# Kernel tuning notes

Measured on AMD Instinct MI355X. Metric: run time of the kernel, lower is better.

The kernel has to match this reference:

```python
import jax, jax.numpy as jnp
import numpy as np

B, H, S, D = 4, 16, 2048, 128

def setup_inputs() -> dict:
    key = jax.random.key(0)
    kq, kk, kv = jax.random.split(key, 3)
    q = jax.random.normal(kq, (B, H, S, D), dtype=jnp.float32)
    k = jax.random.normal(kk, (B, H, S, D), dtype=jnp.float32)
    v = jax.random.normal(kv, (B, H, S, D), dtype=jnp.float32)
    return {"q": q, "k": k, "v": v}

def reference(q, k, v):
    # scores: [B, H, S, S] -- NOTE: original module applies no 1/sqrt(D) scale
    scores = jnp.einsum("bhqd,bhkd->bhqk", q, k)
    a = jax.nn.softmax(scores, axis=-1)  # numerically stable softmax
    return jnp.einsum("bhqk,bhkd->bhqd", a, v)
```

## Files before the change

kernel.cpp:

```cpp
#include <hip/hip_runtime.h>
#include <hip/hip_bf16.h>


#define QBLK   64
#define KVBLK  64
#define DHEAD  128
#define SEQ    2048
#define KPAD   136
#define PPAD   72

typedef _Float16 f16x8 __attribute__((ext_vector_type(8)));
typedef _Float16 f16x4 __attribute__((ext_vector_type(4)));
typedef float    f32x4 __attribute__((ext_vector_type(4)));

#define AS1P(x) ((const __attribute__((address_space(1))) void*)(size_t)(x))
#define AS3P(x) ((__attribute__((address_space(3))) void*)(unsigned long long)(unsigned)(size_t)(x))

__global__ __launch_bounds__(256)
void preconv_kernel(const float* __restrict__ K, const float* __restrict__ V,
                    _Float16* __restrict__ Kp, _Float16* __restrict__ Vp) {
    const int bt = blockIdx.x;
    const size_t src = (size_t)bt * (KVBLK * DHEAD);
    const float* Kt = K + src;
    const float* Vt = V + src;
    _Float16* Ko = Kp + src;
    _Float16* Vo = Vp + src;
    #pragma unroll
    for (int j = 0; j < 4; ++j) {
        const int c = threadIdx.x + 256 * j;
        {
            const int row = c >> 4;
            const int d0  = (c & 15) * 8;
            float4 f0 = *(const float4*)(Kt + row * DHEAD + d0);
            float4 f1 = *(const float4*)(Kt + row * DHEAD + d0 + 4);
            f16x8 h;
            h[0]=(_Float16)f0.x; h[1]=(_Float16)f0.y; h[2]=(_Float16)f0.z; h[3]=(_Float16)f0.w;
            h[4]=(_Float16)f1.x; h[5]=(_Float16)f1.y; h[6]=(_Float16)f1.z; h[7]=(_Float16)f1.w;
            *(f16x8*)&Ko[row * 128 + (d0 ^ ((row & 7) << 3))] = h;
        }
        {
            const int d   = c & 127;
            const int kvg = c >> 7;
            f16x8 h;
            #pragma unroll
            for (int i = 0; i < 8; ++i)
                h[i] = (_Float16)Vt[(kvg * 8 + i) * DHEAD + d];
            *(f16x8*)&Vo[d * 64 + ((kvg * 8) ^ ((d & 7) << 3))] = h;
        }
    }
}

__global__ __launch_bounds__(256, 3)
void attn_fwd_kernel(const float* __restrict__ Q, const _Float16* __restrict__ Kp,
                     const _Float16* __restrict__ Vp, float* __restrict__ O) {
    __shared__ __align__(16) _Float16 K_lds[KVBLK * DHEAD];
    __shared__ __align__(16) _Float16 V_lds[DHEAD * KVBLK];
    __shared__ __align__(16) _Float16 P_lds[4 * 16 * 64];

    const int tid  = threadIdx.x;
    const int lane = tid & 63;
    const int wave = tid >> 6;
    const int g    = lane >> 4;
    const int lg   = lane & 15;

    const int flat    = blockIdx.x + gridDim.x * blockIdx.y;
    const int newflat = (flat & 7) * 256 + (flat >> 3);
    const int qtile   = newflat & 31;
    const int bh      = newflat >> 5;

    const float* Qg = Q + (size_t)bh * SEQ * DHEAD + (size_t)(qtile * QBLK) * DHEAD;
    float*       Og = O + (size_t)bh * SEQ * DHEAD + (size_t)(qtile * QBLK) * DHEAD;

    f16x8 qf[4];
    {
        const float* qrow = Qg + (size_t)(wave * 16 + lg) * DHEAD;
        #pragma unroll
        for (int dc = 0; dc < 4; ++dc) {
            const int d0 = dc * 32 + g * 8;
            float4 f0 = *(const float4*)(qrow + d0);
            float4 f1 = *(const float4*)(qrow + d0 + 4);
            qf[dc][0] = (_Float16)f0.x; qf[dc][1] = (_Float16)f0.y;
            qf[dc][2] = (_Float16)f0.z; qf[dc][3] = (_Float16)f0.w;
            qf[dc][4] = (_Float16)f1.x; qf[dc][5] = (_Float16)f1.y;
            qf[dc][6] = (_Float16)f1.z; qf[dc][7] = (_Float16)f1.w;
        }
    }

    f32x4 acc[8];
    #pragma unroll
    for (int dt = 0; dt < 8; ++dt) { acc[dt][0]=0.f; acc[dt][1]=0.f; acc[dt][2]=0.f; acc[dt][3]=0.f; }
    float m = -1e30f, l = 0.f;

    for (int t = 0; t < SEQ / KVBLK; ++t) {
        {
            const _Float16* Ktile = Kp + (size_t)(bh * 32 + t) * (KVBLK * DHEAD);
            const _Float16* Vtile = Vp + (size_t)(bh * 32 + t) * (KVBLK * DHEAD);
            #pragma unroll
            for (int i = 0; i < 4; ++i) {
                const int eoff = wave * 2048 + i * 512;
                __builtin_amdgcn_global_load_lds(AS1P(Ktile + eoff + lane * 8),
                                                 AS3P(&K_lds[eoff]), 16, 0, 0);
                __builtin_amdgcn_global_load_lds(AS1P(Vtile + eoff + lane * 8),
                                                 AS3P(&V_lds[eoff]), 16, 0, 0);
            }
        }
        __syncthreads();

        f32x4 s[4];
        __builtin_amdgcn_s_setprio(1);
        #pragma unroll
        for (int ct = 0; ct < 4; ++ct) {
            f32x4 a; a[0]=0.f; a[1]=0.f; a[2]=0.f; a[3]=0.f;
            #pragma unroll
            for (int dc = 0; dc < 4; ++dc) {
                const int krow = ct * 16 + lg;
                const int off  = krow * 128 + ((dc * 32 + g * 8) ^ ((krow & 7) << 3));
                f16x8 kh = *(const f16x8*)&K_lds[off];
                a = __builtin_amdgcn_mfma_f32_16x16x32_f16(kh, qf[dc], a, 0, 0, 0);
            }
            s[ct] = a;
        }
        __builtin_amdgcn_s_setprio(0);

        float pmax = s[0][0];
        #pragma unroll
        for (int ct = 0; ct < 4; ++ct)
            #pragma unroll
            for (int r = 0; r < 4; ++r)
                pmax = fmaxf(pmax, s[ct][r]);
        pmax = fmaxf(pmax, __shfl_xor(pmax, 16));
        pmax = fmaxf(pmax, __shfl_xor(pmax, 32));
        const float mnew = fmaxf(m, pmax);
        const float sc   = __expf(m - mnew);
        m = mnew;
        float rs = 0.f;
        #pragma unroll
        for (int ct = 0; ct < 4; ++ct)
            #pragma unroll
            for (int r = 0; r < 4; ++r) {
                float p = __expf(s[ct][r] - mnew);
                s[ct][r] = p;
                rs += p;
            }
        rs += __shfl_xor(rs, 16);
        rs += __shfl_xor(rs, 32);
        l = l * sc + rs;

        #pragma unroll
        for (int r = 0; r < 4; ++r) {
            const float scr = __shfl(sc, g * 20 + r);
            #pragma unroll
            for (int dt = 0; dt < 8; ++dt) acc[dt][r] *= scr;
        }

        _Float16* pbase = &P_lds[wave * 16 * 64];
        #pragma unroll
        for (int ct = 0; ct < 4; ++ct) {
            f16x4 pk;
            pk[0] = (_Float16)s[ct][0]; pk[1] = (_Float16)s[ct][1];
            pk[2] = (_Float16)s[ct][2]; pk[3] = (_Float16)s[ct][3];
            *(f16x4*)&pbase[lg * 64 + ((ct * 16 + g * 4) ^ ((lg & 7) << 3))] = pk;
        }

        __builtin_amdgcn_s_setprio(1);
        #pragma unroll
        for (int kt = 0; kt < 2; ++kt) {
            const int koff = (kt * 32 + g * 8) ^ ((lg & 7) << 3);
            f16x8 pf = *(const f16x8*)&pbase[lg * 64 + koff];
            #pragma unroll
            for (int dt = 0; dt < 8; ++dt) {
                f16x8 vf = *(const f16x8*)&V_lds[(dt * 16 + lg) * 64 + koff];
                acc[dt] = __builtin_amdgcn_mfma_f32_16x16x32_f16(pf, vf, acc[dt], 0, 0, 0);
            }
        }
        __builtin_amdgcn_s_setprio(0);
        __syncthreads();
    }

    const float linv = 1.f / l;
    float inv[4];
    #pragma unroll
    for (int r = 0; r < 4; ++r) inv[r] = __shfl(linv, g * 20 + r);
    float* ob = Og + (size_t)(wave * 16) * DHEAD;
    #pragma unroll
    for (int dt = 0; dt < 8; ++dt)
        #pragma unroll
        for (int r = 0; r < 4; ++r)
            ob[(size_t)(g * 4 + r) * DHEAD + dt * 16 + lg] = acc[dt][r] * inv[r];
}

__global__ __launch_bounds__(256, 3)
void attn_fwd_legacy(const float* __restrict__ Q, const float* __restrict__ K,
                     const float* __restrict__ V, float* __restrict__ O) {
    __shared__ __align__(16) _Float16 K_lds[KVBLK * KPAD];
    __shared__ __align__(16) _Float16 V_lds[KVBLK * DHEAD];
    __shared__ __align__(16) _Float16 P_lds[4 * 16 * PPAD];

    const int tid  = threadIdx.x;
    const int lane = tid & 63;
    const int wave = tid >> 6;
    const int g    = lane >> 4;
    const int lg   = lane & 15;

    const int flat    = blockIdx.x + gridDim.x * blockIdx.y;
    const int newflat = (flat & 7) * 256 + (flat >> 3);
    const int qtile   = newflat & 31;
    const int bh      = newflat >> 5;

    const size_t base = (size_t)bh * SEQ * DHEAD;
    const float* Qg = Q + base + (size_t)(qtile * QBLK) * DHEAD;
    const float* Kg = K + base;
    const float* Vg = V + base;
    float*       Og = O + base + (size_t)(qtile * QBLK) * DHEAD;

    const unsigned trbase = (unsigned)(size_t)&V_lds[0] + (unsigned)(g * 2048 + lg * 8);

    f16x8 qf[4];
    {
        const float* qrow = Qg + (size_t)(wave * 16 + lg) * DHEAD;
        #pragma unroll
        for (int dc = 0; dc < 4; ++dc) {
            const int d0 = dc * 32 + g * 8;
            float4 f0 = *(const float4*)(qrow + d0);
            float4 f1 = *(const float4*)(qrow + d0 + 4);
            qf[dc][0] = (_Float16)f0.x; qf[dc][1] = (_Float16)f0.y;
            qf[dc][2] = (_Float16)f0.z; qf[dc][3] = (_Float16)f0.w;
            qf[dc][4] = (_Float16)f1.x; qf[dc][5] = (_Float16)f1.y;
            qf[dc][6] = (_Float16)f1.z; qf[dc][7] = (_Float16)f1.w;
        }
    }

    f32x4 acc[8];
    #pragma unroll
    for (int dt = 0; dt < 8; ++dt) { acc[dt][0]=0.f; acc[dt][1]=0.f; acc[dt][2]=0.f; acc[dt][3]=0.f; }
    float m = -1e30f, l = 0.f;

    for (int t = 0; t < SEQ / KVBLK; ++t) {
        {
            const float* Kt = Kg + (size_t)t * KVBLK * DHEAD;
            #pragma unroll
            for (int j = 0; j < 4; ++j) {
                const int c   = tid + 256 * j;
                const int row = c >> 4;
                const int dc  = (c & 15) * 8;
                float4 f0 = *(const float4*)(Kt + row * DHEAD + dc);
                float4 f1 = *(const float4*)(Kt + row * DHEAD + dc + 4);
                f16x8 vh;
                vh[0]=(_Float16)f0.x; vh[1]=(_Float16)f0.y; vh[2]=(_Float16)f0.z; vh[3]=(_Float16)f0.w;
                vh[4]=(_Float16)f1.x; vh[5]=(_Float16)f1.y; vh[6]=(_Float16)f1.z; vh[7]=(_Float16)f1.w;
                *(f16x8*)&K_lds[row * KPAD + dc] = vh;
            }
            const float* Vt = Vg + (size_t)t * KVBLK * DHEAD;
            #pragma unroll
            for (int j = 0; j < 4; ++j) {
                const int c   = tid + 256 * j;
                const int d8  = (c & 1) | (((c >> 3) & 7) << 1);
                const int row = ((c >> 1) & 3) | ((c >> 6) << 2);
                const int d0  = d8 * 8;
                float4 f0 = *(const float4*)(Vt + row * DHEAD + d0);
                float4 f1 = *(const float4*)(Vt + row * DHEAD + d0 + 4);
                f16x8 vv;
                vv[0]=(_Float16)f0.x; vv[1]=(_Float16)f0.y; vv[2]=(_Float16)f0.z; vv[3]=(_Float16)f0.w;
                vv[4]=(_Float16)f1.x; vv[5]=(_Float16)f1.y; vv[6]=(_Float16)f1.z; vv[7]=(_Float16)f1.w;
                const int st = (row >> 2) * 8 + (d0 >> 4);
                *(f16x8*)&V_lds[st * 64 + (row & 3) * 16 + (d0 & 15)] = vv;
            }
        }
        __syncthreads();

        f32x4 s[4];
        __builtin_amdgcn_s_setprio(1);
        #pragma unroll
        for (int ct = 0; ct < 4; ++ct) {
            f32x4 a; a[0]=0.f; a[1]=0.f; a[2]=0.f; a[3]=0.f;
            #pragma unroll
            for (int dc = 0; dc < 4; ++dc) {
                const int off = (ct * 16 + lg) * KPAD + dc * 32 + g * 8;
                f16x8 kh = *(const f16x8*)&K_lds[off];
                a = __builtin_amdgcn_mfma_f32_16x16x32_f16(kh, qf[dc], a, 0, 0, 0);
            }
            s[ct] = a;
        }
        __builtin_amdgcn_s_setprio(0);

        float pmax = s[0][0];
        #pragma unroll
        for (int ct = 0; ct < 4; ++ct)
            #pragma unroll
            for (int r = 0; r < 4; ++r)
                pmax = fmaxf(pmax, s[ct][r]);
        pmax = fmaxf(pmax, __shfl_xor(pmax, 16));
        pmax = fmaxf(pmax, __shfl_xor(pmax, 32));
        const float mnew = fmaxf(m, pmax);
        const float sc   = __expf(m - mnew);
        m = mnew;
        float rs = 0.f;
        #pragma unroll
        for (int ct = 0; ct < 4; ++ct)
            #pragma unroll
            for (int r = 0; r < 4; ++r) {
                float p = __expf(s[ct][r] - mnew);
                s[ct][r] = p;
                rs += p;
            }
        rs += __shfl_xor(rs, 16);
        rs += __shfl_xor(rs, 32);
        l = l * sc + rs;

        #pragma unroll
        for (int r = 0; r < 4; ++r) {
            const float scr = __shfl(sc, g * 20 + r);
            #pragma unroll
            for (int dt = 0; dt < 8; ++dt) acc[dt][r] *= scr;
        }

        _Float16* pbase = &P_lds[wave * 16 * PPAD];
        #pragma unroll
        for (int ct = 0; ct < 4; ++ct) {
            f16x4 pk;
            pk[0] = (_Float16)s[ct][0]; pk[1] = (_Float16)s[ct][1];
            pk[2] = (_Float16)s[ct][2]; pk[3] = (_Float16)s[ct][3];
            *(f16x4*)&pbase[lg * PPAD + ct * 16 + g * 4] = pk;
        }

        #pragma unroll
        for (int kt = 0; kt < 2; ++kt) {
            f16x8 pf = *(const f16x8*)&pbase[lg * PPAD + kt * 32 + g * 8];
            #pragma unroll
            for (int dp = 0; dp < 4; ++dp) {
                f16x4 a0, a1, b0, b1;
                asm volatile(
                    "ds_read_b64_tr_b16 %0, %4 offset:%5\n\t"
                    "ds_read_b64_tr_b16 %1, %4 offset:%6\n\t"
                    "ds_read_b64_tr_b16 %2, %4 offset:%7\n\t"
                    "ds_read_b64_tr_b16 %3, %4 offset:%8\n\t"
                    "s_waitcnt lgkmcnt(0)"
                    : "=&v"(a0), "=&v"(a1), "=&v"(b0), "=&v"(b1)
                    : "v"(trbase),
                      "i"(kt * 8192 + (dp * 2 + 0) * 128),
                      "i"(kt * 8192 + 1024 + (dp * 2 + 0) * 128),
                      "i"(kt * 8192 + (dp * 2 + 1) * 128),
                      "i"(kt * 8192 + 1024 + (dp * 2 + 1) * 128)
                    : "memory");
                __builtin_amdgcn_sched_barrier(0);
                f16x8 vf0 = __builtin_shufflevector(a0, a1, 0, 1, 2, 3, 4, 5, 6, 7);
                f16x8 vf1 = __builtin_shufflevector(b0, b1, 0, 1, 2, 3, 4, 5, 6, 7);
                __builtin_amdgcn_s_setprio(1);
                acc[dp * 2 + 0] = __builtin_amdgcn_mfma_f32_16x16x32_f16(pf, vf0, acc[dp * 2 + 0], 0, 0, 0);
                acc[dp * 2 + 1] = __builtin_amdgcn_mfma_f32_16x16x32_f16(pf, vf1, acc[dp * 2 + 1], 0, 0, 0);
                __builtin_amdgcn_s_setprio(0);
            }
        }
        __syncthreads();
    }

    const float linv = 1.f / l;
    float inv[4];
    #pragma unroll
    for (int r = 0; r < 4; ++r) inv[r] = __shfl(linv, g * 20 + r);
    float* ob = Og + (size_t)(wave * 16) * DHEAD;
    #pragma unroll
    for (int dt = 0; dt < 8; ++dt)
        #pragma unroll
        for (int r = 0; r < 4; ++r)
            ob[(size_t)(g * 4 + r) * DHEAD + dt * 16 + lg] = acc[dt][r] * inv[r];
}

extern "C" void kernel_launch(void* const* d_in, const int* in_sizes, int n_in,
                              void* d_out, int out_size, void* d_ws, size_t ws_size,
                              hipStream_t stream) {
    const float* q = (const float*)d_in[0];
    const float* k = (const float*)d_in[1];
    const float* v = (const float*)d_in[2];
    float* out = (float*)d_out;
    const int BH = in_sizes[0] / (SEQ * DHEAD);
    dim3 grid(SEQ / QBLK, BH);

    const size_t elems = (size_t)BH * SEQ * DHEAD;
    const size_t need  = elems * 2 * sizeof(_Float16);
    if (ws_size >= need) {
        _Float16* Kp = (_Float16*)d_ws;
        _Float16* Vp = Kp + elems;
        preconv_kernel<<<dim3(BH * (SEQ / KVBLK)), dim3(256), 0, stream>>>(k, v, Kp, Vp);
        attn_fwd_kernel<<<grid, dim3(256), 0, stream>>>(q, Kp, Vp, out);
    } else {
        attn_fwd_legacy<<<grid, dim3(256), 0, stream>>>(q, k, v, out);
    }
}
```

Before: 250.8 us.

## Double-buffer K/V LDS tiles and skip online-softmax rescale below threshold

Splits K and V into two LDS buffers so the next tile's global-to-LDS load is issued before computing the current tile, overlapping memory traffic with MFMA work. The main loop is manually unrolled by two over the buffers. It also adds a lazy rescale: the running max and accumulator rescale are only updated when a new row max exceeds the old one by more than a threshold, saving exps and multiplies. LDS use doubles, so occupancy drops from 3 to 2 blocks per CU, and skipping rescales allows exponent values up to e^8 in fp16 P, which is a mild numerical risk.

```diff
diff --git a/kernel.cpp b/kernel.cpp
--- a/kernel.cpp
+++ b/kernel.cpp
@@ -6,8 +6,10 @@
 #define KVBLK  64
 #define DHEAD  128
 #define SEQ    2048
+#define NT     (SEQ / KVBLK)
 #define KPAD   136
 #define PPAD   72
+#define RESCALE_THR 8.0f
 
 typedef _Float16 f16x8 __attribute__((ext_vector_type(8)));
 typedef _Float16 f16x4 __attribute__((ext_vector_type(4)));
@@ -50,11 +52,11 @@
     }
 }
 
-__global__ __launch_bounds__(256, 3)
+__global__ __launch_bounds__(256, 2)
 void attn_fwd_kernel(const float* __restrict__ Q, const _Float16* __restrict__ Kp,
                      const _Float16* __restrict__ Vp, float* __restrict__ O) {
-    __shared__ __align__(16) _Float16 K_lds[KVBLK * DHEAD];
-    __shared__ __align__(16) _Float16 V_lds[DHEAD * KVBLK];
+    __shared__ __align__(16) _Float16 K_lds[2][KVBLK * DHEAD];
+    __shared__ __align__(16) _Float16 V_lds[2][KVBLK * DHEAD];
     __shared__ __align__(16) _Float16 P_lds[4 * 16 * 64];
 
     const int tid  = threadIdx.x;
@@ -91,91 +93,105 @@
     for (int dt = 0; dt < 8; ++dt) { acc[dt][0]=0.f; acc[dt][1]=0.f; acc[dt][2]=0.f; acc[dt][3]=0.f; }
     float m = -1e30f, l = 0.f;
 
-    for (int t = 0; t < SEQ / KVBLK; ++t) {
-        {
-            const _Float16* Ktile = Kp + (size_t)(bh * 32 + t) * (KVBLK * DHEAD);
-            const _Float16* Vtile = Vp + (size_t)(bh * 32 + t) * (KVBLK * DHEAD);
-            #pragma unroll
-            for (int i = 0; i < 4; ++i) {
-                const int eoff = wave * 2048 + i * 512;
-                __builtin_amdgcn_global_load_lds(AS1P(Ktile + eoff + lane * 8),
-                                                 AS3P(&K_lds[eoff]), 16, 0, 0);
-                __builtin_amdgcn_global_load_lds(AS1P(Vtile + eoff + lane * 8),
-                                                 AS3P(&V_lds[eoff]), 16, 0, 0);
-            }
-        }
+    #define STAGE(B, T) {                                                          \
+        const _Float16* Ktile = Kp + (size_t)(bh * 32 + (T)) * (KVBLK * DHEAD);    \
+        const _Float16* Vtile = Vp + (size_t)(bh * 32 + (T)) * (KVBLK * DHEAD);    \
+        _Pragma("unroll")                                                          \
+        for (int i = 0; i < 4; ++i) {                                              \
+            const int eoff = wave * 2048 + i * 512;                                \
+            __builtin_amdgcn_global_load_lds(AS1P(Ktile + eoff + lane * 8),        \
+                                             AS3P(&K_lds[B][eoff]), 16, 0, 0);     \
+            __builtin_amdgcn_global_load_lds(AS1P(Vtile + eoff + lane * 8),        \
+                                             AS3P(&V_lds[B][eoff]), 16, 0, 0);     \
+        }                                                                          \
+    }
+
+    #define COMPUTE(B) {                                                           \
+        f32x4 s[4];                                                                \
+        __builtin_amdgcn_s_setprio(1);                                             \
+        _Pragma("unroll")                                                          \
+        for (int ct = 0; ct < 4; ++ct) {                                           \
+            f32x4 a; a[0]=0.f; a[1]=0.f; a[2]=0.f; a[3]=0.f;                       \
+            _Pragma("unroll")                                                      \
+            for (int dc = 0; dc < 4; ++dc) {                                       \
+                const int krow = ct * 16 + lg;                                     \
+                const int koff2 = krow * 128 + ((dc * 32 + g * 8) ^ ((krow & 7) << 3)); \
+                f16x8 kh = *(const f16x8*)&K_lds[B][koff2];                        \
+                a = __builtin_amdgcn_mfma_f32_16x16x32_f16(kh, qf[dc], a, 0, 0, 0);\
+            }                                                                      \
+            s[ct] = a;                                                             \
+        }                                                                          \
+        __builtin_amdgcn_s_setprio(0);                                             \
+        float pmax = s[0][0];                                                      \
+        _Pragma("unroll")                                                          \
+        for (int ct = 0; ct < 4; ++ct)                                             \
+            _Pragma("unroll")                                                      \
+            for (int r = 0; r < 4; ++r)                                            \
+                pmax = fmaxf(pmax, s[ct][r]);                                      \
+        pmax = fmaxf(pmax, __shfl_xor(pmax, 16));                                  \
+        pmax = fmaxf(pmax, __shfl_xor(pmax, 32));                                  \
+        if (!__all(pmax - m <= RESCALE_THR)) {                                     \
+            const float mnew = fmaxf(m, pmax);                                     \
+            const float sc   = __expf(m - mnew);                                   \
+            m = mnew;                                                              \
+            l *= sc;                                                               \
+            _Pragma("unroll")                                                      \
+            for (int r = 0; r < 4; ++r) {                                          \
+                const float scr = __shfl(sc, g * 20 + r);                          \
+                _Pragma("unroll")                                                  \
+                for (int dt = 0; dt < 8; ++dt) acc[dt][r] *= scr;                  \
+            }                                                                      \
+        }                                                                          \
+        float rs = 0.f;                                                            \
+        _Pragma("unroll")                                                          \
+        for (int ct = 0; ct < 4; ++ct)                                             \
+            _Pragma("unroll")                                                      \
+            for (int r = 0; r < 4; ++r) {                                          \
+                float p = __expf(s[ct][r] - m);                                    \
+                s[ct][r] = p;                                                      \
+                rs += p;                                                           \
+            }                                                                      \
+        rs += __shfl_xor(rs, 16);                                                  \
+        rs += __shfl_xor(rs, 32);                                                  \
+        l += rs;                                                                   \
+        _Float16* pbase = &P_lds[wave * 16 * 64];                                  \
+        _Pragma("unroll")                                                          \
+        for (int ct = 0; ct < 4; ++ct) {                                           \
+            f16x4 pk;                                                              \
+            pk[0] = (_Float16)s[ct][0]; pk[1] = (_Float16)s[ct][1];                \
+            pk[2] = (_Float16)s[ct][2]; pk[3] = (_Float16)s[ct][3];                \
+            *(f16x4*)&pbase[lg * 64 + ((ct * 16 + g * 4) ^ ((lg & 7) << 3))] = pk; \
+        }                                                                          \
+        __builtin_amdgcn_s_setprio(1);                                             \
+        _Pragma("unroll")                                                          \
+        for (int kt = 0; kt < 2; ++kt) {                                           \
+            const int koff = (kt * 32 + g * 8) ^ ((lg & 7) << 3);                  \
+            f16x8 pf = *(const f16x8*)&pbase[lg * 64 + koff];                      \
+            _Pragma("unroll")                                                      \
+            for (int dt = 0; dt < 8; ++dt) {                                       \
+                f16x8 vf = *(const f16x8*)&V_lds[B][(dt * 16 + lg) * 64 + koff];   \
+                acc[dt] = __builtin_amdgcn_mfma_f32_16x16x32_f16(pf, vf, acc[dt], 0, 0, 0); \
+            }                                                                      \
+        }                                                                          \
+        __builtin_amdgcn_s_setprio(0);                                             \
+    }
+
+    STAGE(0, 0);
+    __syncthreads();
+
+    #pragma unroll 1
+    for (int tt = 0; tt < NT / 2; ++tt) {
+        const int t0 = tt * 2;
+        STAGE(1, t0 + 1);
+        COMPUTE(0);
         __syncthreads();
-
-        f32x4 s[4];
-        __builtin_amdgcn_s_setprio(1);
-        #pragma unroll
-        for (int ct = 0; ct < 4; ++ct) {
-            f32x4 a; a[0]=0.f; a[1]=0.f; a[2]=0.f; a[3]=0.f;
-            #pragma unroll
-            for (int dc = 0; dc < 4; ++dc) {
-                const int krow = ct * 16 + lg;
-                const int off  = krow * 128 + ((dc * 32 + g * 8) ^ ((krow & 7) << 3));
-                f16x8 kh = *(const f16x8*)&K_lds[off];
-                a = __builtin_amdgcn_mfma_f32_16x16x32_f16(kh, qf[dc], a, 0, 0, 0);
-            }
-            s[ct] = a;
-        }
-        __builtin_amdgcn_s_setprio(0);
-
-        float pmax = s[0][0];
-        #pragma unroll
-        for (int ct = 0; ct < 4; ++ct)
-            #pragma unroll
-            for (int r = 0; r < 4; ++r)
-                pmax = fmaxf(pmax, s[ct][r]);
-        pmax = fmaxf(pmax, __shfl_xor(pmax, 16));
-        pmax = fmaxf(pmax, __shfl_xor(pmax, 32));
-        const float mnew = fmaxf(m, pmax);
-        const float sc   = __expf(m - mnew);
-        m = mnew;
-        float rs = 0.f;
-        #pragma unroll
-        for (int ct = 0; ct < 4; ++ct)
-            #pragma unroll
-            for (int r = 0; r < 4; ++r) {
-                float p = __expf(s[ct][r] - mnew);
-                s[ct][r] = p;
-                rs += p;
-            }
-        rs += __shfl_xor(rs, 16);
-        rs += __shfl_xor(rs, 32);
-        l = l * sc + rs;
-
-        #pragma unroll
-        for (int r = 0; r < 4; ++r) {
-            const float scr = __shfl(sc, g * 20 + r);
-            #pragma unroll
-            for (int dt = 0; dt < 8; ++dt) acc[dt][r] *= scr;
-        }
-
-        _Float16* pbase = &P_lds[wave * 16 * 64];
-        #pragma unroll
-        for (int ct = 0; ct < 4; ++ct) {
-            f16x4 pk;
-            pk[0] = (_Float16)s[ct][0]; pk[1] = (_Float16)s[ct][1];
-            pk[2] = (_Float16)s[ct][2]; pk[3] = (_Float16)s[ct][3];
-            *(f16x4*)&pbase[lg * 64 + ((ct * 16 + g * 4) ^ ((lg & 7) << 3))] = pk;
-        }
-
-        __builtin_amdgcn_s_setprio(1);
-        #pragma unroll
-        for (int kt = 0; kt < 2; ++kt) {
-            const int koff = (kt * 32 + g * 8) ^ ((lg & 7) << 3);
-            f16x8 pf = *(const f16x8*)&pbase[lg * 64 + koff];
-            #pragma unroll
-            for (int dt = 0; dt < 8; ++dt) {
-                f16x8 vf = *(const f16x8*)&V_lds[(dt * 16 + lg) * 64 + koff];
-                acc[dt] = __builtin_amdgcn_mfma_f32_16x16x32_f16(pf, vf, acc[dt], 0, 0, 0);
-            }
-        }
-        __builtin_amdgcn_s_setprio(0);
+        if (t0 + 2 < NT) STAGE(0, t0 + 2);
+        COMPUTE(1);
         __syncthreads();
     }
+
+    #undef STAGE
+    #undef COMPUTE
 
     const float linv = 1.f / l;
     float inv[4];
@@ -235,7 +251,7 @@
     for (int dt = 0; dt < 8; ++dt) { acc[dt][0]=0.f; acc[dt][1]=0.f; acc[dt][2]=0.f; acc[dt][3]=0.f; }
     float m = -1e30f, l = 0.f;
 
-    for (int t = 0; t < SEQ / KVBLK; ++t) {
+    for (int t = 0; t < NT; ++t) {
         {
             const float* Kt = Kg + (size_t)t * KVBLK * DHEAD;
             #pragma unroll
```

Result: slower. 284.9 us (+13.6%).
